# Performance work log

Measured on AMD Instinct MI355X. Metric: run time of the kernel, lower is better.

## Reference

```python
import jax, jax.numpy as jnp
import numpy as np

N_NODES = 100000
N_EDGES = 1600000
IN_DIM = 128
NHID = 128
OUT_DIM = 64


def _gin_layer(x, src, dst, W, b):
    # PyG GINConv with default eps=0: h_i = MLP((1+eps)*x_i + sum_{j->i} x_j)
    # edge_index[0]=src (source/neighbor), edge_index[1]=dst (target)
    agg = jax.ops.segment_sum(x[src], dst, num_segments=N_NODES)  # [N, d]
    return (x + agg) @ W + b


def setup_inputs() -> dict:
    key = jax.random.key(0)
    ks = jax.random.split(key, 8)
    x = jax.random.normal(ks[0], (N_NODES, IN_DIM), dtype=jnp.float32)
    edge_index = jax.random.randint(ks[1], (2, N_EDGES), 0, N_NODES, dtype=jnp.int64)
    # Linear params (kaiming-ish scale)
    W1 = jax.random.normal(ks[2], (IN_DIM, NHID), dtype=jnp.float32) / np.sqrt(IN_DIM)
    b1 = jnp.zeros((NHID,), dtype=jnp.float32)
    Wm = jax.random.normal(ks[3], (NHID, NHID), dtype=jnp.float32) / np.sqrt(NHID)
    bm = jnp.zeros((NHID,), dtype=jnp.float32)
    W2 = jax.random.normal(ks[4], (NHID, OUT_DIM), dtype=jnp.float32) / np.sqrt(NHID)
    b2 = jnp.zeros((OUT_DIM,), dtype=jnp.float32)
    return {"x": x, "edge_index": edge_index, "W1": W1, "b1": b1,
            "Wm": Wm, "bm": bm, "W2": W2, "b2": b2}


def reference(x, edge_index, W1, b1, Wm, bm, W2, b2):
    # Eval-mode forward (dropout is identity when training=False).
    src, dst = edge_index[0], edge_index[1]
    h = jax.nn.relu(_gin_layer(x, src, dst, W1, b1))   # conv1 + relu
    h = jax.nn.relu(_gin_layer(h, src, dst, Wm, bm))   # convx[0] + relu
    out = _gin_layer(h, src, dst, W2, b2)              # conv2 (no relu)
    return out
```

## Files before the change

### kernel.cpp

```cpp
#include <hip/hip_runtime.h>
#include <hip/hip_bf16.h>


#define FEAT 128
#define EPB 16384

typedef unsigned short ushort_t;

__device__ __forceinline__ float bf2f(unsigned int u16) {
    union { unsigned int i; float f; } v;
    v.i = u16 << 16;
    return v.f;
}
__device__ __forceinline__ ushort_t f2bf(float f) {
    union { float f; unsigned int i; } v;
    v.f = f;
    unsigned int x = v.i;
    return (ushort_t)((x + 0x7FFFu + ((x >> 16) & 1u)) >> 16);
}

__global__ __launch_bounds__(64) void detect_i64_kernel(const int* __restrict__ ei,
                                                        int* __restrict__ flag) {
    if (threadIdx.x == 0 && blockIdx.x == 0) {
        int ok = 1;
        for (int t = 0; t < 64; ++t) {
            if (ei[2 * t + 1] != 0) { ok = 0; break; }
        }
        flag[0] = ok;
    }
}

__global__ __launch_bounds__(256) void cast_kernel(const float* __restrict__ X,
                                                   ushort_t* __restrict__ Xb, int total4) {
    for (int i = blockIdx.x * 256 + threadIdx.x; i < total4; i += gridDim.x * 256) {
        float4 v = *(const float4*)(X + (size_t)i * 4);
        ushort4 o;
        o.x = f2bf(v.x); o.y = f2bf(v.y); o.z = f2bf(v.z); o.w = f2bf(v.w);
        *(ushort4*)(Xb + (size_t)i * 4) = o;
    }
}

__global__ __launch_bounds__(256) void phaseA_kernel(const int* __restrict__ ei, int E,
                                                     const int* __restrict__ flag,
                                                     int* __restrict__ G, int NBUCK,
                                                     int NBA) {
    __shared__ int hist[512];
    const int t = threadIdx.x;
    for (int i = t; i < NBUCK; i += 256) hist[i] = 0;
    __syncthreads();
    const int is64 = flag[0];
    const int base = blockIdx.x * EPB;
    const int lim = min(E, base + EPB);
    if (is64) {
        const int2* p = (const int2*)ei;
        for (int e = base + t; e < lim; e += 256) {
            int d = p[(size_t)E + e].x;
            atomicAdd(&hist[d >> 8], 1);
        }
    } else {
        for (int e = base + t; e < lim; e += 256) {
            int d = ei[(size_t)E + e];
            atomicAdd(&hist[d >> 8], 1);
        }
    }
    __syncthreads();
    for (int i = t; i < NBUCK; i += 256) G[i * NBA + blockIdx.x] = hist[i];
}

__global__ __launch_bounds__(1024) void scanG_kernel(const int* __restrict__ G,
                                                     int* __restrict__ Gsc, int M) {
    __shared__ int tot[1024];
    const int t = threadIdx.x;
    const int CH = (M + 1023) / 1024;
    const int lo = t * CH;
    const int hi = min(M, lo + CH);
    int sum = 0;
    for (int i = lo; i < hi; ++i) sum += G[i];
    tot[t] = sum;
    __syncthreads();
    for (int d = 1; d < 1024; d <<= 1) {
        int v = (t >= d) ? tot[t - d] : 0;
        __syncthreads();
        tot[t] += v;
        __syncthreads();
    }
    int run = tot[t] - sum;
    for (int i = lo; i < hi; ++i) {
        int g = G[i];
        Gsc[i] = run;
        run += g;
    }
}

__global__ __launch_bounds__(256) void phaseB_kernel(const int* __restrict__ ei, int E,
                                                     const int* __restrict__ flag,
                                                     const int* __restrict__ Gsc,
                                                     uint2* __restrict__ rec, int NBUCK,
                                                     int NBA) {
    __shared__ int cur[512];
    const int t = threadIdx.x;
    const int blk = blockIdx.x;
    for (int i = t; i < NBUCK; i += 256) cur[i] = Gsc[i * NBA + blk];
    __syncthreads();
    const int is64 = flag[0];
    const int base = blk * EPB;
    const int lim = min(E, base + EPB);
    if (is64) {
        const int2* p = (const int2*)ei;
        for (int e = base + t; e < lim; e += 256) {
            int s = p[e].x;
            int d = p[(size_t)E + e].x;
            int pos = atomicAdd(&cur[d >> 8], 1);
            rec[pos] = make_uint2((unsigned)s, (unsigned)d);
        }
    } else {
        for (int e = base + t; e < lim; e += 256) {
            int s = ei[e];
            int d = ei[(size_t)E + e];
            int pos = atomicAdd(&cur[d >> 8], 1);
            rec[pos] = make_uint2((unsigned)s, (unsigned)d);
        }
    }
}

__global__ __launch_bounds__(256) void phaseC_kernel(const uint2* __restrict__ rec,
                                                     const int* __restrict__ Gsc,
                                                     int* __restrict__ row_start,
                                                     int* __restrict__ col, int N, int E,
                                                     int NBUCK, int NBA) {
    __shared__ int cnt[256];
    __shared__ int scn[256];
    const int b = blockIdx.x;
    const int t = threadIdx.x;
    const int start = Gsc[b * NBA];
    const int end = (b + 1 < NBUCK) ? Gsc[(b + 1) * NBA] : E;
    cnt[t] = 0;
    __syncthreads();
    for (int i = start + t; i < end; i += 256) {
        atomicAdd(&cnt[rec[i].y & 255], 1);
    }
    __syncthreads();
    int c = cnt[t];
    scn[t] = c;
    __syncthreads();
    for (int d = 1; d < 256; d <<= 1) {
        int v = (t >= d) ? scn[t - d] : 0;
        __syncthreads();
        scn[t] += v;
        __syncthreads();
    }
    const int excl = scn[t] - c;
    const int node = b * 256 + t;
    if (node < N) row_start[node] = start + excl;
    if (b == NBUCK - 1 && t == 0) row_start[N] = E;
    cnt[t] = excl;
    __syncthreads();
    for (int i = start + t; i < end; i += 256) {
        uint2 r = rec[i];
        int pos = start + atomicAdd(&cnt[r.y & 255], 1);
        col[pos] = (int)r.x;
    }
}

__global__ __launch_bounds__(256) void agg_bf16_kernel(const ushort_t* __restrict__ Xb,
                                                       const int* __restrict__ row_start,
                                                       const int* __restrict__ col,
                                                       ushort_t* __restrict__ Yb, int N) {
    int w = (blockIdx.x * 256 + threadIdx.x) >> 6;
    int lane = threadIdx.x & 63;
    if (w >= N) return;
    const ushort2* X2 = (const ushort2*)Xb;
    size_t fo = (size_t)w * 64 + lane;
    ushort2 sv = X2[fo];
    float ax = bf2f(sv.x), ay = bf2f(sv.y);
    int s = row_start[w], e = row_start[w + 1];
    int k = s;
    for (; k + 3 < e; k += 4) {
        int j0 = col[k], j1 = col[k + 1], j2 = col[k + 2], j3 = col[k + 3];
        ushort2 v0 = X2[(size_t)j0 * 64 + lane];
        ushort2 v1 = X2[(size_t)j1 * 64 + lane];
        ushort2 v2 = X2[(size_t)j2 * 64 + lane];
        ushort2 v3 = X2[(size_t)j3 * 64 + lane];
        ax += (bf2f(v0.x) + bf2f(v1.x)) + (bf2f(v2.x) + bf2f(v3.x));
        ay += (bf2f(v0.y) + bf2f(v1.y)) + (bf2f(v2.y) + bf2f(v3.y));
    }
    for (; k < e; ++k) {
        ushort2 v = X2[(size_t)col[k] * 64 + lane];
        ax += bf2f(v.x);
        ay += bf2f(v.y);
    }
    ushort2 o;
    o.x = f2bf(ax);
    o.y = f2bf(ay);
    ((ushort2*)Yb)[fo] = o;
}

__global__ __launch_bounds__(256) void mlp_kernel(const ushort_t* __restrict__ A,
                                                  const float* __restrict__ W,
                                                  const float* __restrict__ bias,
                                                  void* __restrict__ C, int M, int NCOL,
                                                  int mode) {
    __shared__ __align__(16) float As[64][68];
    __shared__ __align__(16) float Ws[64][68];
    const int tid = threadIdx.x;
    const int row0 = blockIdx.x * 64;
    const int col0 = blockIdx.y * 64;
    const int tx = tid & 15, ty = tid >> 4;
    const int m0 = ty * 4, n0 = tx * 4;
    float4 acc[4];
#pragma unroll
    for (int i = 0; i < 4; ++i) acc[i] = make_float4(0.f, 0.f, 0.f, 0.f);

    for (int kh = 0; kh < 2; ++kh) {
        const int k0 = kh * 64;
#pragma unroll
        for (int i = 0; i < 2; ++i) {
            int linear = tid + i * 256;
            int m = linear >> 3;
            int ko = (linear & 7) * 8;
            int gm = row0 + m;
            float4 lo = make_float4(0.f, 0.f, 0.f, 0.f);
            float4 hi = make_float4(0.f, 0.f, 0.f, 0.f);
            if (gm < M) {
                uint4 raw = *(const uint4*)(A + (size_t)gm * FEAT + k0 + ko);
                lo.x = bf2f(raw.x & 0xffffu); lo.y = bf2f(raw.x >> 16);
                lo.z = bf2f(raw.y & 0xffffu); lo.w = bf2f(raw.y >> 16);
                hi.x = bf2f(raw.z & 0xffffu); hi.y = bf2f(raw.z >> 16);
                hi.z = bf2f(raw.w & 0xffffu); hi.w = bf2f(raw.w >> 16);
            }
            *(float4*)(&As[m][ko]) = lo;
            *(float4*)(&As[m][ko + 4]) = hi;
        }
#pragma unroll
        for (int i = 0; i < 4; ++i) {
            int linear = tid + i * 256;
            int kk = linear >> 4;
            int nq = linear & 15;
            float4 v = *(const float4*)(W + (size_t)(k0 + kk) * NCOL + col0 + nq * 4);
            *(float4*)(&Ws[kk][nq * 4]) = v;
        }
        __syncthreads();
#pragma unroll 4
        for (int k = 0; k < 64; k += 4) {
            float4 b0 = *(const float4*)(&Ws[k + 0][n0]);
            float4 b1 = *(const float4*)(&Ws[k + 1][n0]);
            float4 b2 = *(const float4*)(&Ws[k + 2][n0]);
            float4 b3 = *(const float4*)(&Ws[k + 3][n0]);
#pragma unroll
            for (int i = 0; i < 4; ++i) {
                float4 a = *(const float4*)(&As[m0 + i][k]);
                acc[i].x += a.x * b0.x + a.y * b1.x + a.z * b2.x + a.w * b3.x;
                acc[i].y += a.x * b0.y + a.y * b1.y + a.z * b2.y + a.w * b3.y;
                acc[i].z += a.x * b0.z + a.y * b1.z + a.z * b2.z + a.w * b3.z;
                acc[i].w += a.x * b0.w + a.y * b1.w + a.z * b2.w + a.w * b3.w;
            }
        }
        __syncthreads();
    }
    float4 bv = *(const float4*)(bias + col0 + n0);
#pragma unroll
    for (int i = 0; i < 4; ++i) {
        int gm = row0 + m0 + i;
        if (gm >= M) continue;
        float4 o;
        o.x = acc[i].x + bv.x;
        o.y = acc[i].y + bv.y;
        o.z = acc[i].z + bv.z;
        o.w = acc[i].w + bv.w;
        if (mode) {
            o.x = fmaxf(o.x, 0.f);
            o.y = fmaxf(o.y, 0.f);
            o.z = fmaxf(o.z, 0.f);
            o.w = fmaxf(o.w, 0.f);
            ushort4 ob;
            ob.x = f2bf(o.x); ob.y = f2bf(o.y); ob.z = f2bf(o.z); ob.w = f2bf(o.w);
            *(ushort4*)((ushort_t*)C + (size_t)gm * NCOL + col0 + n0) = ob;
        } else {
            *(float4*)((float*)C + (size_t)gm * NCOL + col0 + n0) = o;
        }
    }
}

extern "C" void kernel_launch(void* const* d_in, const int* in_sizes, int n_in,
                              void* d_out, int out_size, void* d_ws, size_t ws_size,
                              hipStream_t stream) {
    const float* x = (const float*)d_in[0];
    const int* ei = (const int*)d_in[1];
    const float* W1 = (const float*)d_in[2];
    const float* b1 = (const float*)d_in[3];
    const float* Wm = (const float*)d_in[4];
    const float* bm = (const float*)d_in[5];
    const float* W2 = (const float*)d_in[6];
    const float* b2 = (const float*)d_in[7];
    float* out = (float*)d_out;

    const int N = in_sizes[0] / FEAT;
    const int E = in_sizes[1] / 2;
    const int NHID = FEAT;
    const int OUTD = in_sizes[6] / NHID;

    const int NBA = (E + EPB - 1) / EPB;
    const int NBUCK = (N + 255) >> 8;
    const int M = NBUCK * NBA;

    auto alignup = [](size_t v) { return (v + 255) & ~(size_t)255; };
    char* ws = (char*)d_ws;
    size_t off = 0;
    int* G = (int*)(ws + off);           off += alignup((size_t)M * 4);
    int* Gsc = (int*)(ws + off);         off += alignup((size_t)M * 4);
    int* row_start = (int*)(ws + off);   off += alignup((size_t)(N + 1) * 4);
    int* flag = (int*)(ws + off);        off += 256;
    int* col = (int*)(ws + off);         off += alignup((size_t)E * 4);
    ushort_t* Xb = (ushort_t*)(ws + off); off += alignup((size_t)N * FEAT * 2);
    ushort_t* Yb = (ushort_t*)(ws + off); off += alignup((size_t)N * FEAT * 2);
    ushort_t* Hb = (ushort_t*)(ws + off); off += alignup((size_t)N * FEAT * 2);
    uint2* rec = (uint2*)Yb;
    (void)ws_size;

    cast_kernel<<<2048, 256, 0, stream>>>(x, Xb, N * FEAT / 4);
    detect_i64_kernel<<<1, 64, 0, stream>>>(ei, flag);
    phaseA_kernel<<<NBA, 256, 0, stream>>>(ei, E, flag, G, NBUCK, NBA);
    scanG_kernel<<<1, 1024, 0, stream>>>(G, Gsc, M);
    phaseB_kernel<<<NBA, 256, 0, stream>>>(ei, E, flag, Gsc, rec, NBUCK, NBA);
    phaseC_kernel<<<NBUCK, 256, 0, stream>>>(rec, Gsc, row_start, col, N, E, NBUCK, NBA);

    const int aggBlocks = (N * 64 + 255) / 256;
    dim3 g128((N + 63) / 64, NHID / 64);
    dim3 g64((N + 63) / 64, OUTD / 64);

    agg_bf16_kernel<<<aggBlocks, 256, 0, stream>>>(Xb, row_start, col, Yb, N);
    mlp_kernel<<<g128, 256, 0, stream>>>(Yb, W1, b1, Hb, N, NHID, 1);
    agg_bf16_kernel<<<aggBlocks, 256, 0, stream>>>(Hb, row_start, col, Yb, N);
    mlp_kernel<<<g128, 256, 0, stream>>>(Yb, Wm, bm, Hb, N, NHID, 1);
    agg_bf16_kernel<<<aggBlocks, 256, 0, stream>>>(Hb, row_start, col, Yb, N);
    mlp_kernel<<<g64, 256, 0, stream>>>(Yb, W2, b2, out, N, OUTD, 0);
}
```

Measured before the change: 586.1 us.

## Use half-wave per node in aggregation and larger full-width MLP tiles

The aggregation kernel now assigns 32 lanes per node, each lane loading 4 bf16 values (8 bytes) instead of 2, which halves wavefront count and widens each gather load. The MLP kernel is templated on output width and each block computes 128 rows across all output columns. Each thread accumulates 8 rows by 4 or 8 columns, so the A tile is loaded once instead of once per 64-column slice. This adds register pressure (up to 64 accumulators, with a launch bound asking for 2 blocks per CU) and more LDS per block.

```diff
diff --git a/kernel.cpp b/kernel.cpp
--- a/kernel.cpp
+++ b/kernel.cpp
@@ -166,56 +166,67 @@
                                                        const int* __restrict__ row_start,
                                                        const int* __restrict__ col,
                                                        ushort_t* __restrict__ Yb, int N) {
-    int w = (blockIdx.x * 256 + threadIdx.x) >> 6;
-    int lane = threadIdx.x & 63;
+    int w = (blockIdx.x * 256 + threadIdx.x) >> 5;
+    int l32 = threadIdx.x & 31;
     if (w >= N) return;
-    const ushort2* X2 = (const ushort2*)Xb;
-    size_t fo = (size_t)w * 64 + lane;
-    ushort2 sv = X2[fo];
-    float ax = bf2f(sv.x), ay = bf2f(sv.y);
+    const ushort4* X4 = (const ushort4*)Xb;
+    size_t fo = (size_t)w * 32 + l32;
+    ushort4 sv = X4[fo];
+    float a0 = bf2f(sv.x), a1 = bf2f(sv.y), a2 = bf2f(sv.z), a3 = bf2f(sv.w);
     int s = row_start[w], e = row_start[w + 1];
     int k = s;
     for (; k + 3 < e; k += 4) {
         int j0 = col[k], j1 = col[k + 1], j2 = col[k + 2], j3 = col[k + 3];
-        ushort2 v0 = X2[(size_t)j0 * 64 + lane];
-        ushort2 v1 = X2[(size_t)j1 * 64 + lane];
-        ushort2 v2 = X2[(size_t)j2 * 64 + lane];
-        ushort2 v3 = X2[(size_t)j3 * 64 + lane];
-        ax += (bf2f(v0.x) + bf2f(v1.x)) + (bf2f(v2.x) + bf2f(v3.x));
-        ay += (bf2f(v0.y) + bf2f(v1.y)) + (bf2f(v2.y) + bf2f(v3.y));
+        ushort4 v0 = X4[(size_t)j0 * 32 + l32];
+        ushort4 v1 = X4[(size_t)j1 * 32 + l32];
+        ushort4 v2 = X4[(size_t)j2 * 32 + l32];
+        ushort4 v3 = X4[(size_t)j3 * 32 + l32];
+        a0 += (bf2f(v0.x) + bf2f(v1.x)) + (bf2f(v2.x) + bf2f(v3.x));
+        a1 += (bf2f(v0.y) + bf2f(v1.y)) + (bf2f(v2.y) + bf2f(v3.y));
+        a2 += (bf2f(v0.z) + bf2f(v1.z)) + (bf2f(v2.z) + bf2f(v3.z));
+        a3 += (bf2f(v0.w) + bf2f(v1.w)) + (bf2f(v2.w) + bf2f(v3.w));
     }
     for (; k < e; ++k) {
-        ushort2 v = X2[(size_t)col[k] * 64 + lane];
-        ax += bf2f(v.x);
-        ay += bf2f(v.y);
-    }
-    ushort2 o;
-    o.x = f2bf(ax);
-    o.y = f2bf(ay);
-    ((ushort2*)Yb)[fo] = o;
-}
-
-__global__ __launch_bounds__(256) void mlp_kernel(const ushort_t* __restrict__ A,
-                                                  const float* __restrict__ W,
-                                                  const float* __restrict__ bias,
-                                                  void* __restrict__ C, int M, int NCOL,
-                                                  int mode) {
-    __shared__ __align__(16) float As[64][68];
-    __shared__ __align__(16) float Ws[64][68];
+        ushort4 v = X4[(size_t)col[k] * 32 + l32];
+        a0 += bf2f(v.x);
+        a1 += bf2f(v.y);
+        a2 += bf2f(v.z);
+        a3 += bf2f(v.w);
+    }
+    ushort4 o;
+    o.x = f2bf(a0);
+    o.y = f2bf(a1);
+    o.z = f2bf(a2);
+    o.w = f2bf(a3);
+    ((ushort4*)Yb)[fo] = o;
+}
+
+template <int NT>
+__global__ __launch_bounds__(256, 2) void mlp_kernel(const ushort_t* __restrict__ A,
+                                                     const float* __restrict__ W,
+                                                     const float* __restrict__ bias,
+                                                     void* __restrict__ C, int M, int NCOL,
+                                                     int mode) {
+    constexpr int NBN4 = NT / 64;
+    __shared__ __align__(16) float As[128][68];
+    __shared__ __align__(16) float Ws[64][NT + 4];
     const int tid = threadIdx.x;
-    const int row0 = blockIdx.x * 64;
-    const int col0 = blockIdx.y * 64;
+    const int row0 = blockIdx.x * 128;
     const int tx = tid & 15, ty = tid >> 4;
-    const int m0 = ty * 4, n0 = tx * 4;
-    float4 acc[4];
-#pragma unroll
-    for (int i = 0; i < 4; ++i) acc[i] = make_float4(0.f, 0.f, 0.f, 0.f);
+    const int n0 = tx * (NBN4 * 4);
+
+    float4 accL[8], accH[8];
+#pragma unroll
+    for (int i = 0; i < 8; ++i) {
+        accL[i] = make_float4(0.f, 0.f, 0.f, 0.f);
+        accH[i] = make_float4(0.f, 0.f, 0.f, 0.f);
+    }
 
     for (int kh = 0; kh < 2; ++kh) {
         const int k0 = kh * 64;
 #pragma unroll
-        for (int i = 0; i < 2; ++i) {
-            int linear = tid + i * 256;
+        for (int it = 0; it < 4; ++it) {
+            int linear = tid + it * 256;
             int m = linear >> 3;
             int ko = (linear & 7) * 8;
             int gm = row0 + m;
@@ -232,51 +243,70 @@
             *(float4*)(&As[m][ko + 4]) = hi;
         }
 #pragma unroll
-        for (int i = 0; i < 4; ++i) {
-            int linear = tid + i * 256;
-            int kk = linear >> 4;
-            int nq = linear & 15;
-            float4 v = *(const float4*)(W + (size_t)(k0 + kk) * NCOL + col0 + nq * 4);
+        for (int it = 0; it < NBN4 * 4; ++it) {
+            int linear = tid + it * 256;
+            int kk, nq;
+            if (NT == 128) { kk = linear >> 5; nq = linear & 31; }
+            else           { kk = linear >> 4; nq = linear & 15; }
+            float4 v = *(const float4*)(W + (size_t)(k0 + kk) * NCOL + nq * 4);
             *(float4*)(&Ws[kk][nq * 4]) = v;
         }
         __syncthreads();
-#pragma unroll 4
-        for (int k = 0; k < 64; k += 4) {
-            float4 b0 = *(const float4*)(&Ws[k + 0][n0]);
-            float4 b1 = *(const float4*)(&Ws[k + 1][n0]);
-            float4 b2 = *(const float4*)(&Ws[k + 2][n0]);
-            float4 b3 = *(const float4*)(&Ws[k + 3][n0]);
-#pragma unroll
-            for (int i = 0; i < 4; ++i) {
-                float4 a = *(const float4*)(&As[m0 + i][k]);
-                acc[i].x += a.x * b0.x + a.y * b1.x + a.z * b2.x + a.w * b3.x;
-                acc[i].y += a.x * b0.y + a.y * b1.y + a.z * b2.y + a.w * b3.y;
-                acc[i].z += a.x * b0.z + a.y * b1.z + a.z * b2.z + a.w * b3.z;
-                acc[i].w += a.x * b0.w + a.y * b1.w + a.z * b2.w + a.w * b3.w;
+
+        for (int kc = 0; kc < 64; kc += 4) {
+            float4 a[8];
+#pragma unroll
+            for (int i = 0; i < 8; ++i) a[i] = *(const float4*)(&As[ty + 16 * i][kc]);
+            float4 bL[4], bH[4];
+#pragma unroll
+            for (int j = 0; j < 4; ++j) {
+                bL[j] = *(const float4*)(&Ws[kc + j][n0]);
+                if (NBN4 == 2) bH[j] = *(const float4*)(&Ws[kc + j][n0 + 4]);
             }
-        }
-        __syncthreads();
-    }
-    float4 bv = *(const float4*)(bias + col0 + n0);
-#pragma unroll
-    for (int i = 0; i < 4; ++i) {
-        int gm = row0 + m0 + i;
+#pragma unroll
+            for (int i = 0; i < 8; ++i) {
+                accL[i].x += a[i].x * bL[0].x + a[i].y * bL[1].x + a[i].z * bL[2].x + a[i].w * bL[3].x;
+                accL[i].y += a[i].x * bL[0].y + a[i].y * bL[1].y + a[i].z * bL[2].y + a[i].w * bL[3].y;
+                accL[i].z += a[i].x * bL[0].z + a[i].y * bL[1].z + a[i].z * bL[2].z + a[i].w * bL[3].z;
+                accL[i].w += a[i].x * bL[0].w + a[i].y * bL[1].w + a[i].z * bL[2].w + a[i].w * bL[3].w;
+                if (NBN4 == 2) {
+                    accH[i].x += a[i].x * bH[0].x + a[i].y * bH[1].x + a[i].z * bH[2].x + a[i].w * bH[3].x;
+                    accH[i].y += a[i].x * bH[0].y + a[i].y * bH[1].y + a[i].z * bH[2].y + a[i].w * bH[3].y;
+                    accH[i].z += a[i].x * bH[0].z + a[i].y * bH[1].z + a[i].z * bH[2].z + a[i].w * bH[3].z;
+                    accH[i].w += a[i].x * bH[0].w + a[i].y * bH[1].w + a[i].z * bH[2].w + a[i].w * bH[3].w;
+                }
+            }
+        }
+        __syncthreads();
+    }
+
+    float4 bvL = *(const float4*)(bias + n0);
+    float4 bvH = (NBN4 == 2) ? *(const float4*)(bias + n0 + 4) : make_float4(0.f, 0.f, 0.f, 0.f);
+#pragma unroll
+    for (int i = 0; i < 8; ++i) {
+        int gm = row0 + ty + 16 * i;
         if (gm >= M) continue;
-        float4 o;
-        o.x = acc[i].x + bv.x;
-        o.y = acc[i].y + bv.y;
-        o.z = acc[i].z + bv.z;
-        o.w = acc[i].w + bv.w;
+        float4 oL, oH;
+        oL.x = accL[i].x + bvL.x; oL.y = accL[i].y + bvL.y;
+        oL.z = accL[i].z + bvL.z; oL.w = accL[i].w + bvL.w;
+        oH.x = accH[i].x + bvH.x; oH.y = accH[i].y + bvH.y;
+        oH.z = accH[i].z + bvH.z; oH.w = accH[i].w + bvH.w;
         if (mode) {
-            o.x = fmaxf(o.x, 0.f);
-            o.y = fmaxf(o.y, 0.f);
-            o.z = fmaxf(o.z, 0.f);
-            o.w = fmaxf(o.w, 0.f);
-            ushort4 ob;
-            ob.x = f2bf(o.x); ob.y = f2bf(o.y); ob.z = f2bf(o.z); ob.w = f2bf(o.w);
-            *(ushort4*)((ushort_t*)C + (size_t)gm * NCOL + col0 + n0) = ob;
+            oL.x = fmaxf(oL.x, 0.f); oL.y = fmaxf(oL.y, 0.f);
+            oL.z = fmaxf(oL.z, 0.f); oL.w = fmaxf(oL.w, 0.f);
+            ushort4 obL;
+            obL.x = f2bf(oL.x); obL.y = f2bf(oL.y); obL.z = f2bf(oL.z); obL.w = f2bf(oL.w);
+            *(ushort4*)((ushort_t*)C + (size_t)gm * NCOL + n0) = obL;
+            if (NBN4 == 2) {
+                oH.x = fmaxf(oH.x, 0.f); oH.y = fmaxf(oH.y, 0.f);
+                oH.z = fmaxf(oH.z, 0.f); oH.w = fmaxf(oH.w, 0.f);
+                ushort4 obH;
+                obH.x = f2bf(oH.x); obH.y = f2bf(oH.y); obH.z = f2bf(oH.z); obH.w = f2bf(oH.w);
+                *(ushort4*)((ushort_t*)C + (size_t)gm * NCOL + n0 + 4) = obH;
+            }
         } else {
-            *(float4*)((float*)C + (size_t)gm * NCOL + col0 + n0) = o;
+            *(float4*)((float*)C + (size_t)gm * NCOL + n0) = oL;
+            if (NBN4 == 2) *(float4*)((float*)C + (size_t)gm * NCOL + n0 + 4) = oH;
         }
     }
 }
@@ -324,14 +354,13 @@
     phaseB_kernel<<<NBA, 256, 0, stream>>>(ei, E, flag, Gsc, rec, NBUCK, NBA);
     phaseC_kernel<<<NBUCK, 256, 0, stream>>>(rec, Gsc, row_start, col, N, E, NBUCK, NBA);
 
-    const int aggBlocks = (N * 64 + 255) / 256;
-    dim3 g128((N + 63) / 64, NHID / 64);
-    dim3 g64((N + 63) / 64, OUTD / 64);
+    const int aggBlocks = (N * 32 + 255) / 256;
+    const int mlpBlocks = (N + 127) / 128;
 
     agg_bf16_kernel<<<aggBlocks, 256, 0, stream>>>(Xb, row_start, col, Yb, N);
-    mlp_kernel<<<g128, 256, 0, stream>>>(Yb, W1, b1, Hb, N, NHID, 1);
+    mlp_kernel<128><<<mlpBlocks, 256, 0, stream>>>(Yb, W1, b1, Hb, N, NHID, 1);
     agg_bf16_kernel<<<aggBlocks, 256, 0, stream>>>(Hb, row_start, col, Yb, N);
-    mlp_kernel<<<g128, 256, 0, stream>>>(Yb, Wm, bm, Hb, N, NHID, 1);
+    mlp_kernel<128><<<mlpBlocks, 256, 0, stream>>>(Yb, Wm, bm, Hb, N, NHID, 1);
     agg_bf16_kernel<<<aggBlocks, 256, 0, stream>>>(Hb, row_start, col, Yb, N);
-    mlp_kernel<<<g64, 256, 0, stream>>>(Yb, W2, b2, out, N, OUTD, 0);
-}
+    mlp_kernel<64><<<mlpBlocks, 256, 0, stream>>>(Yb, W2, b2, out, N, OUTD, 0);
+}
```

Measured after the change: 574.8 us. No clear change (-1.9%).
